# Performance work log

Measured on AMD Instinct MI355X. Metric: run time of the kernel, lower is better.

Reference implementation:

```python
import jax, jax.numpy as jnp
import numpy as np

N, E = 50000, 800000
IN_C, HID, OUT_C = 128, 64, 40

def setup_inputs() -> dict:
    key = jax.random.key(0)
    ks = jax.random.split(key, 16)
    def w(k, shape, fan_in):
        return jax.random.normal(k, shape, dtype=jnp.float32) * (1.0 / np.sqrt(fan_in))
    x = jax.random.normal(ks[0], (N, IN_C), dtype=jnp.float32)
    edge_index = jax.random.randint(ks[1], (2, E), 0, N, dtype=jnp.int64)
    return {
        "x": x,
        "edge_index": edge_index,
        "W1": w(ks[2], (IN_C, HID), IN_C), "b1": jnp.zeros((HID,), jnp.float32),
        "W2": w(ks[3], (HID, HID), HID),   "b2": jnp.zeros((HID,), jnp.float32),
        "W3": w(ks[4], (HID, HID), HID),   "b3": jnp.zeros((HID,), jnp.float32),
        "g1": jnp.ones((HID,), jnp.float32), "be1": jnp.zeros((HID,), jnp.float32),
        "g2": jnp.ones((HID,), jnp.float32), "be2": jnp.zeros((HID,), jnp.float32),
        "M1": w(ks[5], (HID, HID), HID),   "mb1": jnp.zeros((HID,), jnp.float32),
        "M2": w(ks[6], (HID, OUT_C), HID), "mb2": jnp.zeros((OUT_C,), jnp.float32),
        "batch_size": N,
    }

def reference(x, edge_index, W1, b1, W2, b2, W3, b3, g1, be1, g2, be2, M1, mb1, M2, mb2, batch_size):
    src, dst = edge_index[0], edge_index[1]
    n = x.shape[0]
    # GCN symmetric norm with self-loops: deg over destination, +1 for self loop
    deg = jax.ops.segment_sum(jnp.ones(src.shape[0], x.dtype), dst, num_segments=n) + 1.0
    dinv = jax.lax.rsqrt(deg)  # deg >= 1 always
    enorm = (dinv[src] * dinv[dst])[:, None]  # [E,1]
    sloop = (dinv * dinv)[:, None]            # [N,1] self-loop norm

    def gcn_conv(h, W, b):
        hw = h @ W                                              # [N,H] transform first
        agg = jax.ops.segment_sum(enorm * hw[src], dst, num_segments=n)
        return agg + sloop * hw + b

    def layer_norm(h, g, be):
        mu = jnp.mean(h, axis=-1, keepdims=True)
        var = jnp.var(h, axis=-1, keepdims=True)
        return (h - mu) * jax.lax.rsqrt(var + 1e-5) * g + be

    h = jax.nn.relu(layer_norm(gcn_conv(x, W1, b1), g1, be1))
    h = jax.nn.relu(layer_norm(gcn_conv(h, W2, b2), g2, be2))
    h = gcn_conv(h, W3, b3)
    # MLP: Linear -> ReLU -> Linear
    h = jax.nn.relu(h @ M1 + mb1) @ M2 + mb2
    return jax.nn.softmax(h[:batch_size], axis=1)
```

## Files before the change

kernel.cpp:

```cpp
#include <hip/hip_runtime.h>
#include <hip/hip_fp16.h>
#include <math.h>

#define HID   64
#define OUTC  40
#define CAP   64

__global__ void zero_kernel(int4* __restrict__ p, int n4) {
    int i = blockIdx.x * blockDim.x + threadIdx.x;
    if (i < n4) p[i] = make_int4(0, 0, 0, 0);
}

__global__ void fill_kernel(const int* __restrict__ src, const int* __restrict__ dst,
                            int* __restrict__ cnt, unsigned short* __restrict__ recs,
                            int E, int N) {
    int g    = blockIdx.x & 7;
    int gblk = blockIdx.x >> 3;
    int nblk = gridDim.x >> 3;
    int slice = (N + 7) >> 3;
    int lo = g * slice;
    int hi = lo + slice; if (hi > N) hi = N;
    for (int e = gblk * blockDim.x + threadIdx.x; e < E; e += nblk * blockDim.x) {
        int d = dst[e];
        if (d >= lo && d < hi) {
            int pos = atomicAdd(&cnt[d], 1);
            if (pos < CAP) recs[(size_t)d * CAP + pos] = (unsigned short)src[e];
        }
    }
}

#define FMA16(acc, a, b) \
    acc[0][0] = fmaf(a.x, b.x, acc[0][0]); acc[0][1] = fmaf(a.x, b.y, acc[0][1]); \
    acc[0][2] = fmaf(a.x, b.z, acc[0][2]); acc[0][3] = fmaf(a.x, b.w, acc[0][3]); \
    acc[1][0] = fmaf(a.y, b.x, acc[1][0]); acc[1][1] = fmaf(a.y, b.y, acc[1][1]); \
    acc[1][2] = fmaf(a.y, b.z, acc[1][2]); acc[1][3] = fmaf(a.y, b.w, acc[1][3]); \
    acc[2][0] = fmaf(a.z, b.x, acc[2][0]); acc[2][1] = fmaf(a.z, b.y, acc[2][1]); \
    acc[2][2] = fmaf(a.z, b.z, acc[2][2]); acc[2][3] = fmaf(a.z, b.w, acc[2][3]); \
    acc[3][0] = fmaf(a.w, b.x, acc[3][0]); acc[3][1] = fmaf(a.w, b.y, acc[3][1]); \
    acc[3][2] = fmaf(a.w, b.z, acc[3][2]); acc[3][3] = fmaf(a.w, b.w, acc[3][3]);

template<int CIN, typename T>
__global__ __launch_bounds__(256) void xform_kernel(const T* __restrict__ X,
                                                    const float* __restrict__ W,
                                                    const int* __restrict__ cnt,
                                                    __half* __restrict__ out, int N) {
    __shared__ float Xs[CIN][68];
    __shared__ float Ws[CIN][68];
    int tid = threadIdx.x;
    int base = blockIdx.x << 6;
    int rows = N - base; if (rows > 64) rows = 64;

    {
        int k = tid >> 4, c = (tid & 15) << 2;
        #pragma unroll
        for (int k0 = 0; k0 < CIN; k0 += 16) {
            float4 wv = *(const float4*)(W + (size_t)((k0 + k) << 6) + c);
            *(float4*)&Ws[k0 + k][c] = wv;
        }
    }
    {
        int r = tid >> 2, q = (tid & 3) << 2;
        int rc = r < rows ? r : 0;
        const T* xp = X + (size_t)(base + rc) * CIN + q;
        #pragma unroll
        for (int k0 = 0; k0 < CIN; k0 += 16) {
            float4 xv;
            if constexpr (sizeof(T) == 4) {
                xv = *(const float4*)(xp + k0);
            } else {
                union { uint2 u; __half2 h[2]; } pk;
                pk.u = *(const uint2*)(xp + k0);
                float2 f01 = __half22float2(pk.h[0]);
                float2 f23 = __half22float2(pk.h[1]);
                xv = make_float4(f01.x, f01.y, f23.x, f23.y);
            }
            Xs[k0 + q + 0][r] = xv.x;
            Xs[k0 + q + 1][r] = xv.y;
            Xs[k0 + q + 2][r] = xv.z;
            Xs[k0 + q + 3][r] = xv.w;
        }
    }
    __syncthreads();

    int tx = tid & 15, ty = tid >> 4;
    float acc[4][4] = {};
    #pragma unroll 4
    for (int k = 0; k < CIN; k++) {
        float4 a = *(const float4*)&Xs[k][ty << 2];
        float4 b = *(const float4*)&Ws[k][tx << 2];
        FMA16(acc, a, b)
    }
    #pragma unroll
    for (int rr = 0; rr < 4; rr++) {
        int row = (ty << 2) + rr;
        if (row < rows) {
            float di = rsqrtf((float)cnt[base + row] + 1.0f);
            union { uint2 u; __half2 h[2]; } pk;
            pk.h[0] = __float22half2_rn(make_float2(acc[rr][0] * di, acc[rr][1] * di));
            pk.h[1] = __float22half2_rn(make_float2(acc[rr][2] * di, acc[rr][3] * di));
            *(uint2*)(out + ((size_t)(base + row) << 6) + (tx << 2)) = pk.u;
        }
    }
    if (blockIdx.x == gridDim.x - 1 && tid < 8) {
        uint4 z = make_uint4(0, 0, 0, 0);
        ((uint4*)(out + ((size_t)N << 6)))[tid] = z;
    }
}

template<bool LN>
__global__ void conv_kernel(const __half* __restrict__ hwh,
                            const unsigned short* __restrict__ recs,
                            const int* __restrict__ cnt,
                            const float* __restrict__ b, const float* __restrict__ g,
                            const float* __restrict__ be, __half* __restrict__ out, int N) {
    int lane = threadIdx.x & 63;
    int row  = (blockIdx.x << 2) + (threadIdx.x >> 6);
    if (row >= N) return;

    int cn = cnt[row];
    int c  = cn > CAP ? CAP : cn;
    int s_l = N;
    if (lane < c) s_l = recs[(size_t)row * CAP + lane];

    int g4 = lane >> 4, j = lane & 15;
    const uint2* hw8 = (const uint2*)hwh;
    float di = rsqrtf((float)cn + 1.0f);
    uint2 selfv = hw8[(size_t)row * 16 + j];

    float acc[4] = {0, 0, 0, 0};
    int kmax = (c + 7) & ~7;
    for (int k = 0; k < kmax; k += 8) {
        int s0 = __shfl(s_l, k + g4), s1 = __shfl(s_l, k + 4 + g4);
        uint2 v0 = hw8[(size_t)s0 * 16 + j];
        uint2 v1 = hw8[(size_t)s1 * 16 + j];
        const __half2* h0 = (const __half2*)&v0;
        const __half2* h1 = (const __half2*)&v1;
        #pragma unroll
        for (int t = 0; t < 2; t++) {
            float2 f0 = __half22float2(h0[t]);
            float2 f1 = __half22float2(h1[t]);
            acc[2*t]   += f0.x + f1.x;
            acc[2*t+1] += f0.y + f1.y;
        }
    }
    #pragma unroll
    for (int off = 16; off < 64; off <<= 1) {
        #pragma unroll
        for (int t = 0; t < 4; t++) acc[t] += __shfl_xor(acc[t], off);
    }

    int f0 = j << 2;
    const __half2* sp = (const __half2*)&selfv;
    float4 bb = *(const float4*)(b + f0);
    {
        float2 fa = __half22float2(sp[0]);
        float2 fb = __half22float2(sp[1]);
        acc[0] = fmaf(di, acc[0] + fa.x, bb.x);
        acc[1] = fmaf(di, acc[1] + fa.y, bb.y);
        acc[2] = fmaf(di, acc[2] + fb.x, bb.z);
        acc[3] = fmaf(di, acc[3] + fb.y, bb.w);
    }

    if (LN) {
        float s = (acc[0] + acc[1]) + (acc[2] + acc[3]);
        #pragma unroll
        for (int o = 1; o < 16; o <<= 1) s += __shfl_xor(s, o);
        float mu = s * (1.f / 64.f);
        float v = 0.f;
        #pragma unroll
        for (int t = 0; t < 4; t++) { acc[t] -= mu; v += acc[t] * acc[t]; }
        #pragma unroll
        for (int o = 1; o < 16; o <<= 1) v += __shfl_xor(v, o);
        float r = rsqrtf(v * (1.f / 64.f) + 1e-5f);
        float4 gg = *(const float4*)(g + f0);
        float4 eb = *(const float4*)(be + f0);
        acc[0] = fmaxf(fmaf(acc[0] * r, gg.x, eb.x), 0.f);
        acc[1] = fmaxf(fmaf(acc[1] * r, gg.y, eb.y), 0.f);
        acc[2] = fmaxf(fmaf(acc[2] * r, gg.z, eb.z), 0.f);
        acc[3] = fmaxf(fmaf(acc[3] * r, gg.w, eb.w), 0.f);
    }
    if (g4 == 0) {
        union { uint2 u; __half2 h[2]; } pk;
        pk.h[0] = __float22half2_rn(make_float2(acc[0], acc[1]));
        pk.h[1] = __float22half2_rn(make_float2(acc[2], acc[3]));
        *(uint2*)(out + (size_t)row * 64 + f0) = pk.u;
    }
}

__global__ __launch_bounds__(256) void mlp_kernel(const __half* __restrict__ h,
                           const float* __restrict__ M1, const float* __restrict__ mb1,
                           const float* __restrict__ M2, const float* __restrict__ mb2,
                           float* __restrict__ out, int N) {
    __shared__ float Hs [64][68];
    __shared__ float W1s[64][68];
    __shared__ float H2s[64][68];
    __shared__ float W2s[64][44];
    int tid = threadIdx.x;
    int base = blockIdx.x << 6;
    int rows = N - base; if (rows > 64) rows = 64;

    {
        int k = tid >> 4, c = (tid & 15) << 2;
        #pragma unroll
        for (int k0 = 0; k0 < 64; k0 += 16) {
            float4 wv = *(const float4*)(M1 + (size_t)((k0 + k) << 6) + c);
            *(float4*)&W1s[k0 + k][c] = wv;
        }
    }
    for (int i = tid; i < 64 * OUTC; i += 256)
        W2s[i / OUTC][i % OUTC] = M2[i];
    {
        int r = tid >> 2, q = (tid & 3) << 2;
        int rc = r < rows ? r : 0;
        const __half* xp = h + (((size_t)(base + rc)) << 6) + q;
        #pragma unroll
        for (int k0 = 0; k0 < 64; k0 += 16) {
            union { uint2 u; __half2 hh[2]; } pk;
            pk.u = *(const uint2*)(xp + k0);
            float2 f01 = __half22float2(pk.hh[0]);
            float2 f23 = __half22float2(pk.hh[1]);
            Hs[k0 + q + 0][r] = f01.x;
            Hs[k0 + q + 1][r] = f01.y;
            Hs[k0 + q + 2][r] = f23.x;
            Hs[k0 + q + 3][r] = f23.y;
        }
    }
    __syncthreads();

    int tx = tid & 15, ty = tid >> 4;

    float acc[4][4] = {};
    #pragma unroll 4
    for (int k = 0; k < 64; k++) {
        float4 a = *(const float4*)&Hs[k][ty << 2];
        float4 b = *(const float4*)&W1s[k][tx << 2];
        FMA16(acc, a, b)
    }
    float4 b1v = *(const float4*)(mb1 + (tx << 2));
    #pragma unroll
    for (int cc = 0; cc < 4; cc++) {
        float bc = cc == 0 ? b1v.x : cc == 1 ? b1v.y : cc == 2 ? b1v.z : b1v.w;
        #pragma unroll
        for (int rr = 0; rr < 4; rr++)
            H2s[(tx << 2) + cc][(ty << 2) + rr] = fmaxf(acc[rr][cc] + bc, 0.f);
    }
    __syncthreads();

    int bx = (tx < 10) ? (tx << 2) : 0;
    float acc2[4][4] = {};
    #pragma unroll 4
    for (int k = 0; k < 64; k++) {
        float4 a = *(const float4*)&H2s[k][ty << 2];
        float4 b = *(const float4*)&W2s[k][bx];
        FMA16(acc2, a, b)
    }
    float4 b2v = *(const float4*)(mb2 + bx);

    #pragma unroll
    for (int rr = 0; rr < 4; rr++) {
        float v0 = acc2[rr][0] + b2v.x, v1 = acc2[rr][1] + b2v.y;
        float v2 = acc2[rr][2] + b2v.z, v3 = acc2[rr][3] + b2v.w;
        float m = fmaxf(fmaxf(v0, v1), fmaxf(v2, v3));
        if (tx >= 10) m = -1e30f;
        #pragma unroll
        for (int s = 1; s < 16; s <<= 1) m = fmaxf(m, __shfl_xor(m, s));
        float e0 = __expf(v0 - m), e1 = __expf(v1 - m);
        float e2 = __expf(v2 - m), e3 = __expf(v3 - m);
        float sum = (tx < 10) ? (e0 + e1) + (e2 + e3) : 0.f;
        #pragma unroll
        for (int s = 1; s < 16; s <<= 1) sum += __shfl_xor(sum, s);
        float inv = 1.f / sum;
        int row = (ty << 2) + rr;
        if (tx < 10 && row < rows)
            *(float4*)(out + (size_t)(base + row) * OUTC + bx) =
                make_float4(e0 * inv, e1 * inv, e2 * inv, e3 * inv);
    }
}

extern "C" void kernel_launch(void* const* d_in, const int* in_sizes, int n_in,
                              void* d_out, int out_size, void* d_ws, size_t ws_size,
                              hipStream_t stream) {
    const float* x   = (const float*)d_in[0];
    const int*   ei  = (const int*)  d_in[1];
    const float* W1  = (const float*)d_in[2];
    const float* b1  = (const float*)d_in[3];
    const float* W2  = (const float*)d_in[4];
    const float* b2  = (const float*)d_in[5];
    const float* W3  = (const float*)d_in[6];
    const float* b3  = (const float*)d_in[7];
    const float* g1  = (const float*)d_in[8];
    const float* be1 = (const float*)d_in[9];
    const float* g2  = (const float*)d_in[10];
    const float* be2 = (const float*)d_in[11];
    const float* M1  = (const float*)d_in[12];
    const float* mb1 = (const float*)d_in[13];
    const float* M2  = (const float*)d_in[14];
    const float* mb2 = (const float*)d_in[15];

    const int IN_C = 128;
    int N = in_sizes[0] / IN_C;
    int E = in_sizes[1] / 2;
    const int* src = ei;
    const int* dst = ei + E;

    char* ws = (char*)d_ws;
    size_t off = 0;
    auto carve = [&](size_t bytes) -> void* {
        void* p = ws + off;
        off = (off + bytes + 255) & ~(size_t)255;
        return p;
    };
    int*            cnt  = (int*)           carve(((size_t)N + 4) * sizeof(int));
    unsigned short* recs = (unsigned short*)carve((size_t)N * CAP * sizeof(unsigned short));
    __half*         HWh  = (__half*)        carve((size_t)(N + 1) * HID * sizeof(__half));
    __half*         H    = (__half*)        carve((size_t)(N + 1) * HID * sizeof(__half));
    __half*         PH   = (__half*)        carve((size_t)(N + 1) * HID * sizeof(__half));

    int n4 = (N + 3) / 4;
    zero_kernel<<<(n4 + 255) / 256, 256, 0, stream>>>((int4*)cnt, n4);

    int rb = (N + 3) / 4;
    int tb = (N + 63) / 64;

    fill_kernel<<<2048, 256, 0, stream>>>(src, dst, cnt, recs, E, N);

    xform_kernel<128, float><<<tb, 256, 0, stream>>>(x, W1, cnt, HWh, N);
    conv_kernel<true><<<rb, 256, 0, stream>>>(HWh, recs, cnt, b1, g1, be1, H, N);
    xform_kernel<64, __half><<<tb, 256, 0, stream>>>(H, W2, cnt, HWh, N);
    conv_kernel<true><<<rb, 256, 0, stream>>>(HWh, recs, cnt, b2, g2, be2, H, N);
    xform_kernel<64, __half><<<tb, 256, 0, stream>>>(H, W3, cnt, HWh, N);
    conv_kernel<false><<<rb, 256, 0, stream>>>(HWh, recs, cnt, b3, nullptr, nullptr, PH, N);

    mlp_kernel<<<tb, 256, 0, stream>>>(PH, M1, mb1, M2, mb2, (float*)d_out, N);
}
```

Before: 187.2 us.

## Fold W3 and M1 into one matrix, removing the first MLP GEMM

Because aggregation is linear, conv3 followed by M1 equals aggregating h@(W3·M1) and adding b3·M1+mb1. A small kernel precomputes W3M1 and the fused bias, the third xform uses it, and the third conv applies ReLU. The MLP kernel now only does the M2 GEMM and softmax, which cuts shared memory and one 64x64 GEMM per row. The cost is an extra tiny launch and slightly different rounding, since the fused product is stored in fp16 before ReLU.

```diff
diff --git a/kernel.cpp b/kernel.cpp
--- a/kernel.cpp
+++ b/kernel.cpp
@@ -26,6 +26,41 @@
             int pos = atomicAdd(&cnt[d], 1);
             if (pos < CAP) recs[(size_t)d * CAP + pos] = (unsigned short)src[e];
         }
+    }
+}
+
+__global__ __launch_bounds__(256) void w3m1_kernel(const float* __restrict__ W3,
+                                                   const float* __restrict__ M1,
+                                                   const float* __restrict__ b3,
+                                                   const float* __restrict__ mb1,
+                                                   float* __restrict__ W3M1,
+                                                   float* __restrict__ b31) {
+    __shared__ float M1s[64][68];
+    int tid = threadIdx.x;
+    {
+        int k = tid >> 4, c = (tid & 15) << 2;
+        #pragma unroll
+        for (int k0 = 0; k0 < 64; k0 += 16)
+            *(float4*)&M1s[k0 + k][c] = *(const float4*)(M1 + ((size_t)(k0 + k) << 6) + c);
+    }
+    __syncthreads();
+    int row = (blockIdx.x << 4) + (tid >> 4);
+    int c4  = (tid & 15) << 2;
+    float a0 = 0.f, a1 = 0.f, a2 = 0.f, a3 = 0.f;
+    const float* wr = W3 + ((size_t)row << 6);
+    #pragma unroll 4
+    for (int j = 0; j < 64; j++) {
+        float w = wr[j];
+        float4 m = *(const float4*)&M1s[j][c4];
+        a0 = fmaf(w, m.x, a0); a1 = fmaf(w, m.y, a1);
+        a2 = fmaf(w, m.z, a2); a3 = fmaf(w, m.w, a3);
+    }
+    *(float4*)(W3M1 + ((size_t)row << 6) + c4) = make_float4(a0, a1, a2, a3);
+    if (blockIdx.x == 0 && tid < 64) {
+        float acc = mb1[tid];
+        #pragma unroll 4
+        for (int k = 0; k < 64; k++) acc = fmaf(b3[k], M1s[k][tid], acc);
+        b31[tid] = acc;
     }
 }
 
@@ -107,7 +142,7 @@
     }
 }
 
-template<bool LN>
+template<bool LN, bool RELU>
 __global__ void conv_kernel(const __half* __restrict__ hwh,
                             const unsigned short* __restrict__ recs,
                             const int* __restrict__ cnt,
@@ -178,6 +213,9 @@
         acc[1] = fmaxf(fmaf(acc[1] * r, gg.y, eb.y), 0.f);
         acc[2] = fmaxf(fmaf(acc[2] * r, gg.z, eb.z), 0.f);
         acc[3] = fmaxf(fmaf(acc[3] * r, gg.w, eb.w), 0.f);
+    } else if (RELU) {
+        #pragma unroll
+        for (int t = 0; t < 4; t++) acc[t] = fmaxf(acc[t], 0.f);
     }
     if (g4 == 0) {
         union { uint2 u; __half2 h[2]; } pk;
@@ -188,25 +226,14 @@
 }
 
 __global__ __launch_bounds__(256) void mlp_kernel(const __half* __restrict__ h,
-                           const float* __restrict__ M1, const float* __restrict__ mb1,
                            const float* __restrict__ M2, const float* __restrict__ mb2,
                            float* __restrict__ out, int N) {
     __shared__ float Hs [64][68];
-    __shared__ float W1s[64][68];
-    __shared__ float H2s[64][68];
     __shared__ float W2s[64][44];
     int tid = threadIdx.x;
     int base = blockIdx.x << 6;
     int rows = N - base; if (rows > 64) rows = 64;
 
-    {
-        int k = tid >> 4, c = (tid & 15) << 2;
-        #pragma unroll
-        for (int k0 = 0; k0 < 64; k0 += 16) {
-            float4 wv = *(const float4*)(M1 + (size_t)((k0 + k) << 6) + c);
-            *(float4*)&W1s[k0 + k][c] = wv;
-        }
-    }
     for (int i = tid; i < 64 * OUTC; i += 256)
         W2s[i / OUTC][i % OUTC] = M2[i];
     {
@@ -228,29 +255,11 @@
     __syncthreads();
 
     int tx = tid & 15, ty = tid >> 4;
-
-    float acc[4][4] = {};
-    #pragma unroll 4
-    for (int k = 0; k < 64; k++) {
-        float4 a = *(const float4*)&Hs[k][ty << 2];
-        float4 b = *(const float4*)&W1s[k][tx << 2];
-        FMA16(acc, a, b)
-    }
-    float4 b1v = *(const float4*)(mb1 + (tx << 2));
-    #pragma unroll
-    for (int cc = 0; cc < 4; cc++) {
-        float bc = cc == 0 ? b1v.x : cc == 1 ? b1v.y : cc == 2 ? b1v.z : b1v.w;
-        #pragma unroll
-        for (int rr = 0; rr < 4; rr++)
-            H2s[(tx << 2) + cc][(ty << 2) + rr] = fmaxf(acc[rr][cc] + bc, 0.f);
-    }
-    __syncthreads();
-
     int bx = (tx < 10) ? (tx << 2) : 0;
     float acc2[4][4] = {};
     #pragma unroll 4
     for (int k = 0; k < 64; k++) {
-        float4 a = *(const float4*)&H2s[k][ty << 2];
+        float4 a = *(const float4*)&Hs[k][ty << 2];
         float4 b = *(const float4*)&W2s[k][bx];
         FMA16(acc2, a, b)
     }
@@ -314,7 +323,9 @@
     unsigned short* recs = (unsigned short*)carve((size_t)N * CAP * sizeof(unsigned short));
     __half*         HWh  = (__half*)        carve((size_t)(N + 1) * HID * sizeof(__half));
     __half*         H    = (__half*)        carve((size_t)(N + 1) * HID * sizeof(__half));
-    __half*         PH   = (__half*)        carve((size_t)(N + 1) * HID * sizeof(__half));
+    __half*         H3   = (__half*)        carve((size_t)(N + 1) * HID * sizeof(__half));
+    float*          W3M1 = (float*)         carve((size_t)HID * HID * sizeof(float));
+    float*          b31  = (float*)         carve((size_t)HID * sizeof(float));
 
     int n4 = (N + 3) / 4;
     zero_kernel<<<(n4 + 255) / 256, 256, 0, stream>>>((int4*)cnt, n4);
@@ -323,13 +334,14 @@
     int tb = (N + 63) / 64;
 
     fill_kernel<<<2048, 256, 0, stream>>>(src, dst, cnt, recs, E, N);
+    w3m1_kernel<<<4, 256, 0, stream>>>(W3, M1, b3, mb1, W3M1, b31);
 
     xform_kernel<128, float><<<tb, 256, 0, stream>>>(x, W1, cnt, HWh, N);
-    conv_kernel<true><<<rb, 256, 0, stream>>>(HWh, recs, cnt, b1, g1, be1, H, N);
+    conv_kernel<true, false><<<rb, 256, 0, stream>>>(HWh, recs, cnt, b1, g1, be1, H, N);
     xform_kernel<64, __half><<<tb, 256, 0, stream>>>(H, W2, cnt, HWh, N);
-    conv_kernel<true><<<rb, 256, 0, stream>>>(HWh, recs, cnt, b2, g2, be2, H, N);
-    xform_kernel<64, __half><<<tb, 256, 0, stream>>>(H, W3, cnt, HWh, N);
-    conv_kernel<false><<<rb, 256, 0, stream>>>(HWh, recs, cnt, b3, nullptr, nullptr, PH, N);
-
-    mlp_kernel<<<tb, 256, 0, stream>>>(PH, M1, mb1, M2, mb2, (float*)d_out, N);
-}
+    conv_kernel<true, false><<<rb, 256, 0, stream>>>(HWh, recs, cnt, b2, g2, be2, H, N);
+    xform_kernel<64, __half><<<tb, 256, 0, stream>>>(H, W3M1, cnt, HWh, N);
+    conv_kernel<false, true><<<rb, 256, 0, stream>>>(HWh, recs, cnt, b31, nullptr, nullptr, H3, N);
+
+    mlp_kernel<<<tb, 256, 0, stream>>>(H3, M2, mb2, (float*)d_out, N);
+}
```

New measurement: 182.5 us. -2.5%, faster.
